# Performance work log

Measured on AMD Instinct MI355X. Metric: run time of the kernel, lower is better.

The kernel has to match this reference:

```python
import jax, jax.numpy as jnp
import numpy as np

N = 100000   # nodes
E = 1600000  # edges (avg degree 16)
D = 128      # input channels
H = 128      # hidden channels
BN_EPS = 1e-5

def setup_inputs() -> dict:
    key = jax.random.key(0)
    ks = jax.random.split(key, 8)
    x = jax.random.normal(ks[0], (N, D), dtype=jnp.float32)
    edge_index = jax.random.randint(ks[1], (2, E), 0, N, dtype=jnp.int32)
    s = 0.02
    W1 = jax.random.normal(ks[2], (D, H), dtype=jnp.float32) * s
    b1 = jnp.zeros((H,), jnp.float32)
    g1 = jnp.ones((H,), jnp.float32)   # BN gamma
    be1 = jnp.zeros((H,), jnp.float32) # BN beta
    W2 = jax.random.normal(ks[3], (H, H), dtype=jnp.float32) * s
    b2 = jnp.zeros((H,), jnp.float32)
    g2 = jnp.ones((H,), jnp.float32)
    be2 = jnp.zeros((H,), jnp.float32)
    eps = jnp.zeros((), jnp.float32)   # trainable GIN eps, init 0
    return {"x": x, "edge_index": edge_index, "W1": W1, "b1": b1, "g1": g1,
            "be1": be1, "W2": W2, "b2": b2, "g2": g2, "be2": be2, "eps": eps}

def _bn_relu(h, gamma, beta):
    # BatchNorm1d in training mode: biased batch statistics over the node dim
    mu = jnp.mean(h, axis=0)
    var = jnp.mean(jnp.square(h - mu), axis=0)
    return jax.nn.relu((h - mu) * jax.lax.rsqrt(var + BN_EPS) * gamma + beta)

def reference(x, edge_index, W1, b1, g1, be1, W2, b2, g2, be2, eps):
    src, dst = edge_index[0], edge_index[1]
    # GIN neighbor aggregation: scatter-add of source features onto destinations
    agg = jax.ops.segment_sum(x[src], dst, num_segments=x.shape[0])  # [N, D]
    h = (1.0 + eps) * x + agg
    # 2-layer MLP: Linear -> BN -> ReLU, twice
    h = _bn_relu(h @ W1 + b1, g1, be1)
    h = _bn_relu(h @ W2 + b2, g2, be2)
    return h
```

## Files before the change

kernel.cpp:

```cpp
#include <hip/hip_runtime.h>

#define DIM 128
#define BINSHIFT 7
#define BINSZ 128
#define BCAP 2560
#define EPB 8192

typedef __attribute__((ext_vector_type(8))) short bf16x8;
typedef __attribute__((ext_vector_type(4))) float f32x4;

__device__ inline unsigned short f2b(float f) {
    unsigned u = __builtin_bit_cast(unsigned, f);
    unsigned r = (u + 0x7FFFu + ((u >> 16) & 1u)) >> 16;
    return (unsigned short)r;
}
__device__ inline float b2f(unsigned short h) {
    unsigned u = ((unsigned)h) << 16;
    return __builtin_bit_cast(float, u);
}

__global__ __launch_bounds__(256)
void init_gcur(unsigned* __restrict__ gcur, int nbins)
{
    int i = blockIdx.x * 256 + threadIdx.x;
    if (i < nbins) gcur[i] = (unsigned)i * BCAP;
}

__global__ __launch_bounds__(256)
void x_to_bf16(const float* __restrict__ x, unsigned short* __restrict__ xb, int n8)
{
    int i = blockIdx.x * 256 + threadIdx.x;
    if (i >= n8) return;
    float4 a = ((const float4*)x)[i * 2];
    float4 b = ((const float4*)x)[i * 2 + 1];
    bf16x8 o;
    o[0] = (short)f2b(a.x); o[1] = (short)f2b(a.y); o[2] = (short)f2b(a.z); o[3] = (short)f2b(a.w);
    o[4] = (short)f2b(b.x); o[5] = (short)f2b(b.y); o[6] = (short)f2b(b.z); o[7] = (short)f2b(b.w);
    ((bf16x8*)xb)[i] = o;
}

__global__ __launch_bounds__(1024)
void bin_edges(const int* __restrict__ src, const int* __restrict__ dst,
               unsigned* __restrict__ gcur, unsigned* __restrict__ binned,
               int E, int nbins)
{
    __shared__ unsigned hist[1024];
    __shared__ unsigned base[1024];
    const int t = threadIdx.x;
    const long long bb = (long long)blockIdx.x * EPB;
    if (t < nbins) hist[t] = 0;
    __syncthreads();

    unsigned pk[8], pos[8];
    int bn[8];
    bool ok[8];
    #pragma unroll
    for (int i = 0; i < 8; ++i) {
        long long idx = bb + i * 1024 + t;
        ok[i] = idx < E;
        if (ok[i]) {
            int s = src[idx], d = dst[idx];
            pk[i] = ((unsigned)(d & (BINSZ - 1)) << 17) | (unsigned)s;
            bn[i] = d >> BINSHIFT;
            pos[i] = atomicAdd(&hist[bn[i]], 1u);
        }
    }
    __syncthreads();
    if (t < nbins) base[t] = atomicAdd(&gcur[t], hist[t]);
    __syncthreads();
    #pragma unroll
    for (int i = 0; i < 8; ++i) {
        if (ok[i]) {
            unsigned off = base[bn[i]] + pos[i];
            if (off < (unsigned)(bn[i] + 1) * BCAP) binned[off] = pk[i];
        }
    }
}

__global__ __launch_bounds__(512)
void bin_agg2(const unsigned short* __restrict__ xb, const float* __restrict__ epsp,
              const unsigned* __restrict__ gcur, const unsigned* __restrict__ binned,
              unsigned short* __restrict__ h0b, int N)
{
    __shared__ unsigned sorted[BCAP];
    __shared__ unsigned hist[BINSZ];
    __shared__ unsigned base[BINSZ];
    __shared__ unsigned cur[BINSZ];
    const int t = threadIdx.x;
    const int bin = blockIdx.x;
    const int node0 = bin << BINSHIFT;

    if (t < BINSZ) hist[t] = 0;
    __syncthreads();

    int cnt = (int)gcur[bin] - bin * BCAP;
    if (cnt > BCAP) cnt = BCAP;
    const unsigned* __restrict__ bp = binned + (size_t)bin * BCAP;

    for (int i = t; i < cnt; i += 512)
        atomicAdd(&hist[(bp[i] >> 17) & (BINSZ - 1)], 1u);
    __syncthreads();
    if (t == 0) {
        unsigned run = 0;
        for (int i = 0; i < BINSZ; ++i) { base[i] = run; run += hist[i]; }
    }
    __syncthreads();
    if (t < BINSZ) cur[t] = base[t];
    __syncthreads();
    for (int i = t; i < cnt; i += 512) {
        unsigned p = bp[i];
        unsigned pos = atomicAdd(&cur[(p >> 17) & (BINSZ - 1)], 1u);
        sorted[pos] = p & 0x1FFFFu;
    }
    __syncthreads();

    const float e = 1.0f + epsp[0];
    const int g = (t & 15) * 8;
    const int slot = t >> 4;
    #pragma unroll
    for (int sw = 0; sw < 4; ++sw) {
        int dn = sw * 32 + slot;
        int node = node0 + dn;
        if (node < N) {
            bf16x8 v0 = *(const bf16x8*)(xb + (size_t)node * DIM + g);
            float acc[8];
            #pragma unroll
            for (int q = 0; q < 8; ++q) acc[q] = e * b2f((unsigned short)v0[q]);
            const int b0 = (int)base[dn], hn = (int)hist[dn];
            int j = 0;
            for (; j + 4 <= hn; j += 4) {
                unsigned s0 = sorted[b0 + j + 0];
                unsigned s1 = sorted[b0 + j + 1];
                unsigned s2 = sorted[b0 + j + 2];
                unsigned s3 = sorted[b0 + j + 3];
                bf16x8 r0 = *(const bf16x8*)(xb + (size_t)s0 * DIM + g);
                bf16x8 r1 = *(const bf16x8*)(xb + (size_t)s1 * DIM + g);
                bf16x8 r2 = *(const bf16x8*)(xb + (size_t)s2 * DIM + g);
                bf16x8 r3 = *(const bf16x8*)(xb + (size_t)s3 * DIM + g);
                #pragma unroll
                for (int q = 0; q < 8; ++q)
                    acc[q] += b2f((unsigned short)r0[q]) + b2f((unsigned short)r1[q])
                            + b2f((unsigned short)r2[q]) + b2f((unsigned short)r3[q]);
            }
            for (; j < hn; ++j) {
                unsigned s0 = sorted[b0 + j];
                bf16x8 r0 = *(const bf16x8*)(xb + (size_t)s0 * DIM + g);
                #pragma unroll
                for (int q = 0; q < 8; ++q) acc[q] += b2f((unsigned short)r0[q]);
            }
            bf16x8 o;
            #pragma unroll
            for (int q = 0; q < 8; ++q) o[q] = (short)f2b(acc[q]);
            *(bf16x8*)(h0b + (size_t)node * DIM + g) = o;
        }
    }
}

template<bool APPLY_BN, bool OUT_BF16>
__global__ __launch_bounds__(1024)
void gemm_mfma(const unsigned short* __restrict__ A, const float* __restrict__ Wf,
               const float* __restrict__ bias, const float* __restrict__ ss,
               void* __restrict__ outp, float* __restrict__ stats, int N)
{
    __shared__ unsigned short sWT[128 * 128];
    __shared__ float red[256];
    const int tid = threadIdx.x;

    #pragma unroll
    for (int i = 0; i < 4; ++i) {
        int idx = (i * 1024 + tid) * 4;
        float4 w = *(const float4*)&Wf[idx];
        int k = idx >> 7, n0 = idx & 127;
        sWT[(n0 + 0) * 128 + (k ^ (((n0 + 0) & 7) << 3))] = f2b(w.x);
        sWT[(n0 + 1) * 128 + (k ^ (((n0 + 1) & 7) << 3))] = f2b(w.y);
        sWT[(n0 + 2) * 128 + (k ^ (((n0 + 2) & 7) << 3))] = f2b(w.z);
        sWT[(n0 + 3) * 128 + (k ^ (((n0 + 3) & 7) << 3))] = f2b(w.w);
    }
    if (tid < 256) red[tid] = 0.f;
    __syncthreads();

    const int lane = tid & 63;
    const int wave = tid >> 6;
    const int r0   = blockIdx.x * 256 + wave * 16;
    const int rl   = lane & 15;
    const int kg   = lane >> 4;
    int rr = r0 + rl;
    int rclamp = rr < N ? rr : N - 1;
    const unsigned short* arow = A + (size_t)rclamp * DIM + kg * 8;

    f32x4 acc[8];
    #pragma unroll
    for (int nt = 0; nt < 8; ++nt) acc[nt] = (f32x4)(0.f);

    #pragma unroll
    for (int kk = 0; kk < 128; kk += 32) {
        bf16x8 a8 = *(const bf16x8*)(arow + kk);
        if (APPLY_BN) {
            const float* sc = ss + kk + kg * 8;
            const float* sh = sc + DIM;
            bf16x8 tt;
            #pragma unroll
            for (int j = 0; j < 8; ++j) {
                float f = b2f((unsigned short)a8[j]) * sc[j] + sh[j];
                tt[j] = (short)f2b(fmaxf(f, 0.f));
            }
            a8 = tt;
        }
        const int ks = kk + kg * 8;
        #pragma unroll
        for (int nt = 0; nt < 8; ++nt) {
            int n = nt * 16 + rl;
            bf16x8 b8 = *(const bf16x8*)&sWT[n * 128 + (ks ^ ((n & 7) << 3))];
            acc[nt] = __builtin_amdgcn_mfma_f32_16x16x32_bf16(a8, b8, acc[nt], 0, 0, 0);
        }
    }

    const int orow0 = r0 + kg * 4;
    #pragma unroll
    for (int nt = 0; nt < 8; ++nt) {
        int n = nt * 16 + rl;
        float bb = bias[n];
        float ls = 0.f, ls2 = 0.f;
        #pragma unroll
        for (int j = 0; j < 4; ++j) {
            int r = orow0 + j;
            if (r < N) {
                float v = acc[nt][j] + bb;
                if (OUT_BF16) ((unsigned short*)outp)[(size_t)r * DIM + n] = f2b(v);
                else          ((float*)outp)[(size_t)r * DIM + n] = v;
                ls += v; ls2 += v * v;
            }
        }
        ls  += __shfl_xor(ls, 16);  ls  += __shfl_xor(ls, 32);
        ls2 += __shfl_xor(ls2, 16); ls2 += __shfl_xor(ls2, 32);
        if (kg == 0) { atomicAdd(&red[n], ls); atomicAdd(&red[128 + n], ls2); }
    }
    __syncthreads();
    if (tid < 256) atomicAdd(&stats[tid], red[tid]);
}

__global__ void bn_finalize(const float* __restrict__ stats, const float* __restrict__ gamma,
                            const float* __restrict__ beta, float* __restrict__ ss, float invN)
{
    int c = threadIdx.x;
    float mu  = stats[c] * invN;
    float var = stats[DIM + c] * invN - mu * mu;
    var = fmaxf(var, 0.f);
    float sc = gamma[c] * rsqrtf(var + 1e-5f);
    ss[c]       = sc;
    ss[DIM + c] = beta[c] - mu * sc;
}

__global__ __launch_bounds__(256)
void bn_relu_out(float* __restrict__ h, const float* __restrict__ ss, int n4)
{
    int i = blockIdx.x * 256 + threadIdx.x;
    if (i >= n4) return;
    int c = (i * 4) & 127;
    float4 sc = *(const float4*)&ss[c];
    float4 sh = *(const float4*)&ss[DIM + c];
    float4 v = ((float4*)h)[i];
    v.x = fmaxf(v.x * sc.x + sh.x, 0.f);
    v.y = fmaxf(v.y * sc.y + sh.y, 0.f);
    v.z = fmaxf(v.z * sc.z + sh.z, 0.f);
    v.w = fmaxf(v.w * sc.w + sh.w, 0.f);
    ((float4*)h)[i] = v;
}

extern "C" void kernel_launch(void* const* d_in, const int* in_sizes, int n_in,
                              void* d_out, int out_size, void* d_ws, size_t ws_size,
                              hipStream_t stream) {
    const float* x    = (const float*)d_in[0];
    const int*   ei   = (const int*)  d_in[1];
    const float* W1   = (const float*)d_in[2];
    const float* b1   = (const float*)d_in[3];
    const float* g1   = (const float*)d_in[4];
    const float* be1  = (const float*)d_in[5];
    const float* W2   = (const float*)d_in[6];
    const float* b2   = (const float*)d_in[7];
    const float* g2   = (const float*)d_in[8];
    const float* be2  = (const float*)d_in[9];
    const float* epsp = (const float*)d_in[10];
    float* out = (float*)d_out;

    const int N = in_sizes[0] / DIM;
    const int E = in_sizes[1] / 2;
    const int* src = ei;
    const int* dst = ei + E;
    const int nbins = (N + BINSZ - 1) >> BINSHIFT;

    unsigned short* xb  = (unsigned short*)d_ws;
    unsigned short* h0b = xb + (size_t)N * DIM;
    unsigned short* regC = h0b + (size_t)N * DIM;
    unsigned* binned = (unsigned*)regC;
    unsigned short* h1b = regC;
    unsigned* gcur = (unsigned*)(regC + (size_t)N * DIM);
    float* stats1 = (float*)(gcur + 1024);
    float* stats2 = stats1 + 256;
    float* ss1    = stats2 + 256;
    float* ss2    = ss1 + 256;

    hipMemsetAsync(stats1, 0, 512 * sizeof(float), stream);
    init_gcur<<<(nbins + 255) / 256, 256, 0, stream>>>(gcur, nbins);

    const int n8 = N * DIM / 8;
    x_to_bf16<<<(n8 + 255) / 256, 256, 0, stream>>>(x, xb, n8);

    bin_edges<<<(E + EPB - 1) / EPB, 1024, 0, stream>>>(src, dst, gcur, binned, E, nbins);
    bin_agg2<<<nbins, 512, 0, stream>>>(xb, epsp, gcur, binned, h0b, N);

    const int gblocks = (N + 255) / 256;
    gemm_mfma<false, true><<<gblocks, 1024, 0, stream>>>(h0b, W1, b1, nullptr, h1b, stats1, N);
    bn_finalize<<<1, DIM, 0, stream>>>(stats1, g1, be1, ss1, 1.0f / (float)N);
    gemm_mfma<true, false><<<gblocks, 1024, 0, stream>>>(h1b, W2, b2, ss1, out, stats2, N);
    bn_finalize<<<1, DIM, 0, stream>>>(stats2, g2, be2, ss2, 1.0f / (float)N);
    const int n4 = N * DIM / 4;
    bn_relu_out<<<(n4 + 255) / 256, 256, 0, stream>>>(out, ss2, n4);
}
```

Measured before the change: 191.5 us.

## Slice bf16 features by channel and split aggregation into sort plus sliced gather

Converts x into eight channel-slice arrays so that each gather block reads only one 32-byte slice per neighbor. The hope is that each slice's working set (about 3.2MB) stays resident in cache across random source indices. Per-bin sorting moves into its own kernel that writes sorted indices, bases and histograms to global memory, and the gather runs with eight blocks per bin. The second GEMM now writes a bf16 intermediate that a final BN+ReLU pass expands to fp32, halving that round trip, at the cost of bf16 rounding before the last normalization. gcur initialization is also replaced by a memset.

```diff
diff --git a/kernel.cpp b/kernel.cpp
--- a/kernel.cpp
+++ b/kernel.cpp
@@ -5,6 +5,8 @@
 #define BINSZ 128
 #define BCAP 2560
 #define EPB 8192
+#define NSL 8
+#define SC 16
 
 typedef __attribute__((ext_vector_type(8))) short bf16x8;
 typedef __attribute__((ext_vector_type(4))) float f32x4;
@@ -20,23 +22,24 @@
 }
 
 __global__ __launch_bounds__(256)
-void init_gcur(unsigned* __restrict__ gcur, int nbins)
-{
-    int i = blockIdx.x * 256 + threadIdx.x;
-    if (i < nbins) gcur[i] = (unsigned)i * BCAP;
-}
-
-__global__ __launch_bounds__(256)
-void x_to_bf16(const float* __restrict__ x, unsigned short* __restrict__ xb, int n8)
-{
-    int i = blockIdx.x * 256 + threadIdx.x;
-    if (i >= n8) return;
-    float4 a = ((const float4*)x)[i * 2];
-    float4 b = ((const float4*)x)[i * 2 + 1];
-    bf16x8 o;
-    o[0] = (short)f2b(a.x); o[1] = (short)f2b(a.y); o[2] = (short)f2b(a.z); o[3] = (short)f2b(a.w);
-    o[4] = (short)f2b(b.x); o[5] = (short)f2b(b.y); o[6] = (short)f2b(b.z); o[7] = (short)f2b(b.w);
-    ((bf16x8*)xb)[i] = o;
+void x_to_slices(const float* __restrict__ x, unsigned short* __restrict__ xbs, int N)
+{
+    int t = blockIdx.x * 256 + threadIdx.x;
+    if (t >= N * NSL) return;
+    int node = t >> 3, s = t & 7;
+    const float* xp = x + (size_t)node * DIM + s * SC;
+    float4 a = *(const float4*)(xp + 0);
+    float4 b = *(const float4*)(xp + 4);
+    float4 c = *(const float4*)(xp + 8);
+    float4 d = *(const float4*)(xp + 12);
+    unsigned short* o = xbs + ((size_t)s * N + node) * SC;
+    bf16x8 o0, o1;
+    o0[0]=(short)f2b(a.x); o0[1]=(short)f2b(a.y); o0[2]=(short)f2b(a.z); o0[3]=(short)f2b(a.w);
+    o0[4]=(short)f2b(b.x); o0[5]=(short)f2b(b.y); o0[6]=(short)f2b(b.z); o0[7]=(short)f2b(b.w);
+    o1[0]=(short)f2b(c.x); o1[1]=(short)f2b(c.y); o1[2]=(short)f2b(c.z); o1[3]=(short)f2b(c.w);
+    o1[4]=(short)f2b(d.x); o1[5]=(short)f2b(d.y); o1[6]=(short)f2b(d.z); o1[7]=(short)f2b(d.w);
+    *(bf16x8*)(o + 0) = o0;
+    *(bf16x8*)(o + 8) = o1;
 }
 
 __global__ __launch_bounds__(1024)
@@ -66,7 +69,7 @@
         }
     }
     __syncthreads();
-    if (t < nbins) base[t] = atomicAdd(&gcur[t], hist[t]);
+    if (t < nbins) base[t] = (unsigned)t * BCAP + atomicAdd(&gcur[t], hist[t]);
     __syncthreads();
     #pragma unroll
     for (int i = 0; i < 8; ++i) {
@@ -78,22 +81,20 @@
 }
 
 __global__ __launch_bounds__(512)
-void bin_agg2(const unsigned short* __restrict__ xb, const float* __restrict__ epsp,
-              const unsigned* __restrict__ gcur, const unsigned* __restrict__ binned,
-              unsigned short* __restrict__ h0b, int N)
-{
-    __shared__ unsigned sorted[BCAP];
+void bin_sort(const unsigned* __restrict__ gcur, const unsigned* __restrict__ binned,
+              unsigned* __restrict__ srt, unsigned* __restrict__ gbase,
+              unsigned* __restrict__ ghist)
+{
     __shared__ unsigned hist[BINSZ];
     __shared__ unsigned base[BINSZ];
     __shared__ unsigned cur[BINSZ];
     const int t = threadIdx.x;
     const int bin = blockIdx.x;
-    const int node0 = bin << BINSHIFT;
 
     if (t < BINSZ) hist[t] = 0;
     __syncthreads();
 
-    int cnt = (int)gcur[bin] - bin * BCAP;
+    int cnt = (int)gcur[bin];
     if (cnt > BCAP) cnt = BCAP;
     const unsigned* __restrict__ bp = binned + (size_t)bin * BCAP;
 
@@ -107,53 +108,80 @@
     __syncthreads();
     if (t < BINSZ) cur[t] = base[t];
     __syncthreads();
+    unsigned* __restrict__ sp = srt + (size_t)bin * BCAP;
     for (int i = t; i < cnt; i += 512) {
         unsigned p = bp[i];
         unsigned pos = atomicAdd(&cur[(p >> 17) & (BINSZ - 1)], 1u);
-        sorted[pos] = p & 0x1FFFFu;
+        sp[pos] = p & 0x1FFFFu;
+    }
+    if (t < BINSZ) {
+        gbase[bin * BINSZ + t] = base[t];
+        ghist[bin * BINSZ + t] = hist[t];
+    }
+}
+
+__global__ __launch_bounds__(256)
+void gather_slice(const unsigned short* __restrict__ xbs, const float* __restrict__ epsp,
+                  const unsigned* __restrict__ gcur, const unsigned* __restrict__ srt,
+                  const unsigned* __restrict__ gbase, const unsigned* __restrict__ ghist,
+                  unsigned short* __restrict__ h0b, int N)
+{
+    __shared__ unsigned ssrt[BCAP];
+    __shared__ unsigned sbase[BINSZ];
+    __shared__ unsigned shist[BINSZ];
+    const int t = threadIdx.x;
+    const int bin = blockIdx.x >> 3;
+    const int slice = blockIdx.x & 7;
+    const int node0 = bin << BINSHIFT;
+
+    int cnt = (int)gcur[bin];
+    if (cnt > BCAP) cnt = BCAP;
+    const unsigned* __restrict__ sp = srt + (size_t)bin * BCAP;
+    for (int i = t; i < cnt; i += 256) ssrt[i] = sp[i];
+    if (t < BINSZ) {
+        sbase[t] = gbase[bin * BINSZ + t];
+        shist[t] = ghist[bin * BINSZ + t];
     }
     __syncthreads();
 
     const float e = 1.0f + epsp[0];
-    const int g = (t & 15) * 8;
-    const int slot = t >> 4;
-    #pragma unroll
-    for (int sw = 0; sw < 4; ++sw) {
-        int dn = sw * 32 + slot;
-        int node = node0 + dn;
-        if (node < N) {
-            bf16x8 v0 = *(const bf16x8*)(xb + (size_t)node * DIM + g);
-            float acc[8];
-            #pragma unroll
-            for (int q = 0; q < 8; ++q) acc[q] = e * b2f((unsigned short)v0[q]);
-            const int b0 = (int)base[dn], hn = (int)hist[dn];
-            int j = 0;
-            for (; j + 4 <= hn; j += 4) {
-                unsigned s0 = sorted[b0 + j + 0];
-                unsigned s1 = sorted[b0 + j + 1];
-                unsigned s2 = sorted[b0 + j + 2];
-                unsigned s3 = sorted[b0 + j + 3];
-                bf16x8 r0 = *(const bf16x8*)(xb + (size_t)s0 * DIM + g);
-                bf16x8 r1 = *(const bf16x8*)(xb + (size_t)s1 * DIM + g);
-                bf16x8 r2 = *(const bf16x8*)(xb + (size_t)s2 * DIM + g);
-                bf16x8 r3 = *(const bf16x8*)(xb + (size_t)s3 * DIM + g);
-                #pragma unroll
-                for (int q = 0; q < 8; ++q)
-                    acc[q] += b2f((unsigned short)r0[q]) + b2f((unsigned short)r1[q])
-                            + b2f((unsigned short)r2[q]) + b2f((unsigned short)r3[q]);
-            }
-            for (; j < hn; ++j) {
-                unsigned s0 = sorted[b0 + j];
-                bf16x8 r0 = *(const bf16x8*)(xb + (size_t)s0 * DIM + g);
-                #pragma unroll
-                for (int q = 0; q < 8; ++q) acc[q] += b2f((unsigned short)r0[q]);
-            }
-            bf16x8 o;
-            #pragma unroll
-            for (int q = 0; q < 8; ++q) o[q] = (short)f2b(acc[q]);
-            *(bf16x8*)(h0b + (size_t)node * DIM + g) = o;
-        }
-    }
+    const int dn = t >> 1;
+    const int c8 = (t & 1) * 8;
+    const int node = node0 + dn;
+    if (node >= N) return;
+
+    const unsigned short* __restrict__ xs = xbs + (size_t)slice * N * SC + c8;
+    bf16x8 v0 = *(const bf16x8*)(xs + (size_t)node * SC);
+    float acc[8];
+    #pragma unroll
+    for (int q = 0; q < 8; ++q) acc[q] = e * b2f((unsigned short)v0[q]);
+
+    const int b0 = (int)sbase[dn], hn = (int)shist[dn];
+    int j = 0;
+    for (; j + 4 <= hn; j += 4) {
+        unsigned s0 = ssrt[b0 + j + 0];
+        unsigned s1 = ssrt[b0 + j + 1];
+        unsigned s2 = ssrt[b0 + j + 2];
+        unsigned s3 = ssrt[b0 + j + 3];
+        bf16x8 r0 = *(const bf16x8*)(xs + (size_t)s0 * SC);
+        bf16x8 r1 = *(const bf16x8*)(xs + (size_t)s1 * SC);
+        bf16x8 r2 = *(const bf16x8*)(xs + (size_t)s2 * SC);
+        bf16x8 r3 = *(const bf16x8*)(xs + (size_t)s3 * SC);
+        #pragma unroll
+        for (int q = 0; q < 8; ++q)
+            acc[q] += b2f((unsigned short)r0[q]) + b2f((unsigned short)r1[q])
+                    + b2f((unsigned short)r2[q]) + b2f((unsigned short)r3[q]);
+    }
+    for (; j < hn; ++j) {
+        unsigned s0 = ssrt[b0 + j];
+        bf16x8 r0 = *(const bf16x8*)(xs + (size_t)s0 * SC);
+        #pragma unroll
+        for (int q = 0; q < 8; ++q) acc[q] += b2f((unsigned short)r0[q]);
+    }
+    bf16x8 o;
+    #pragma unroll
+    for (int q = 0; q < 8; ++q) o[q] = (short)f2b(acc[q]);
+    *(bf16x8*)(h0b + (size_t)node * DIM + slice * SC + c8) = o;
 }
 
 template<bool APPLY_BN, bool OUT_BF16>
@@ -252,19 +280,24 @@
 }
 
 __global__ __launch_bounds__(256)
-void bn_relu_out(float* __restrict__ h, const float* __restrict__ ss, int n4)
+void bn_relu_out_b(const unsigned short* __restrict__ h2b, const float* __restrict__ ss,
+                   float* __restrict__ out, int n8)
 {
     int i = blockIdx.x * 256 + threadIdx.x;
-    if (i >= n4) return;
-    int c = (i * 4) & 127;
-    float4 sc = *(const float4*)&ss[c];
-    float4 sh = *(const float4*)&ss[DIM + c];
-    float4 v = ((float4*)h)[i];
-    v.x = fmaxf(v.x * sc.x + sh.x, 0.f);
-    v.y = fmaxf(v.y * sc.y + sh.y, 0.f);
-    v.z = fmaxf(v.z * sc.z + sh.z, 0.f);
-    v.w = fmaxf(v.w * sc.w + sh.w, 0.f);
-    ((float4*)h)[i] = v;
+    if (i >= n8) return;
+    int c = (i * 8) & 127;
+    bf16x8 v = *(const bf16x8*)(h2b + (size_t)i * 8);
+    float4 o0, o1;
+    o0.x = fmaxf(b2f((unsigned short)v[0]) * ss[c+0] + ss[DIM+c+0], 0.f);
+    o0.y = fmaxf(b2f((unsigned short)v[1]) * ss[c+1] + ss[DIM+c+1], 0.f);
+    o0.z = fmaxf(b2f((unsigned short)v[2]) * ss[c+2] + ss[DIM+c+2], 0.f);
+    o0.w = fmaxf(b2f((unsigned short)v[3]) * ss[c+3] + ss[DIM+c+3], 0.f);
+    o1.x = fmaxf(b2f((unsigned short)v[4]) * ss[c+4] + ss[DIM+c+4], 0.f);
+    o1.y = fmaxf(b2f((unsigned short)v[5]) * ss[c+5] + ss[DIM+c+5], 0.f);
+    o1.z = fmaxf(b2f((unsigned short)v[6]) * ss[c+6] + ss[DIM+c+6], 0.f);
+    o1.w = fmaxf(b2f((unsigned short)v[7]) * ss[c+7] + ss[DIM+c+7], 0.f);
+    ((float4*)out)[i * 2 + 0] = o0;
+    ((float4*)out)[i * 2 + 1] = o1;
 }
 
 extern "C" void kernel_launch(void* const* d_in, const int* in_sizes, int n_in,
@@ -289,31 +322,34 @@
     const int* dst = ei + E;
     const int nbins = (N + BINSZ - 1) >> BINSHIFT;
 
-    unsigned short* xb  = (unsigned short*)d_ws;
-    unsigned short* h0b = xb + (size_t)N * DIM;
-    unsigned short* regC = h0b + (size_t)N * DIM;
-    unsigned* binned = (unsigned*)regC;
-    unsigned short* h1b = regC;
-    unsigned* gcur = (unsigned*)(regC + (size_t)N * DIM);
+    const size_t SZ = (size_t)N * DIM * sizeof(unsigned short);
+    char* w = (char*)d_ws;
+    unsigned short* xbs = (unsigned short*)w;
+    unsigned short* h1b = xbs;
+    unsigned short* h0b = (unsigned short*)(w + SZ);
+    unsigned short* h2b = h0b;
+    unsigned* binned = (unsigned*)(w + 2 * SZ);
+    unsigned* srt    = binned + (size_t)nbins * BCAP;
+    unsigned* gbase  = srt + (size_t)nbins * BCAP;
+    unsigned* ghist  = gbase + (size_t)nbins * BINSZ;
+    unsigned* gcur   = ghist + (size_t)nbins * BINSZ;
     float* stats1 = (float*)(gcur + 1024);
     float* stats2 = stats1 + 256;
     float* ss1    = stats2 + 256;
     float* ss2    = ss1 + 256;
 
-    hipMemsetAsync(stats1, 0, 512 * sizeof(float), stream);
-    init_gcur<<<(nbins + 255) / 256, 256, 0, stream>>>(gcur, nbins);
-
-    const int n8 = N * DIM / 8;
-    x_to_bf16<<<(n8 + 255) / 256, 256, 0, stream>>>(x, xb, n8);
-
+    hipMemsetAsync(gcur, 0, (1024 + 512) * sizeof(unsigned), stream);
+
+    x_to_slices<<<(N * NSL + 255) / 256, 256, 0, stream>>>(x, xbs, N);
     bin_edges<<<(E + EPB - 1) / EPB, 1024, 0, stream>>>(src, dst, gcur, binned, E, nbins);
-    bin_agg2<<<nbins, 512, 0, stream>>>(xb, epsp, gcur, binned, h0b, N);
+    bin_sort<<<nbins, 512, 0, stream>>>(gcur, binned, srt, gbase, ghist);
+    gather_slice<<<nbins * NSL, 256, 0, stream>>>(xbs, epsp, gcur, srt, gbase, ghist, h0b, N);
 
     const int gblocks = (N + 255) / 256;
     gemm_mfma<false, true><<<gblocks, 1024, 0, stream>>>(h0b, W1, b1, nullptr, h1b, stats1, N);
     bn_finalize<<<1, DIM, 0, stream>>>(stats1, g1, be1, ss1, 1.0f / (float)N);
-    gemm_mfma<true, false><<<gblocks, 1024, 0, stream>>>(h1b, W2, b2, ss1, out, stats2, N);
+    gemm_mfma<true, true><<<gblocks, 1024, 0, stream>>>(h1b, W2, b2, ss1, h2b, stats2, N);
     bn_finalize<<<1, DIM, 0, stream>>>(stats2, g2, be2, ss2, 1.0f / (float)N);
-    const int n4 = N * DIM / 4;
-    bn_relu_out<<<(n4 + 255) / 256, 256, 0, stream>>>(out, ss2, n4);
-}
+    const int n8 = N * DIM / 8;
+    bn_relu_out_b<<<(n8 + 255) / 256, 256, 0, stream>>>(h2b, ss2, out, n8);
+}
```

New measurement: 203.3 us. +6.2%, slower.
